# Kernel tuning notes

Hardware: AMD Instinct MI355X
Metric: run time of the kernel (lower is better)

The kernel has to match this reference:

```python
import jax, jax.numpy as jnp
import numpy as np

N, E, HN, K = 4096, 8192, 1024, 8
NF, EF = 128, 64
NH = [256, 256]
EH = [64, 64]
EMB = NH[-1] + len(EH)  # 258
BN_EPS = 1e-5


def setup_inputs() -> dict:
    key = jax.random.key(0)
    ks = jax.random.split(key, 16)

    def nrm(k, shape, fan):
        return jax.random.normal(k, shape, jnp.float32) / np.float32(np.sqrt(fan))

    return {
        "X_n": jax.random.normal(ks[0], (N, NF), jnp.float32),
        "X_e": jax.random.normal(ks[1], (E, EF), jnp.float32),
        # row-normalized-ish adjacency and scaled Laplacian to keep activations bounded
        "A_tilde": jax.random.uniform(ks[2], (N, N), jnp.float32) / np.float32(N),
        "L1_tilde": jax.random.normal(ks[3], (E, E), jnp.float32) / np.float32(np.sqrt(E)),
        "B1": jax.random.normal(ks[4], (N, E), jnp.float32) / np.float32(np.sqrt(E)),
        # GNN params (Linear stores weight as [out, in])
        "gnn_W1": nrm(ks[5], (NH[0], NF), NF), "gnn_b1": jnp.zeros((NH[0],), jnp.float32),
        "gnn_W2": nrm(ks[6], (NH[1], NH[0]), NH[0]), "gnn_b2": jnp.zeros((NH[1],), jnp.float32),
        # HoSC layer 1: in=EF, out=EH[0]
        "hosc_W1": nrm(ks[7], (EH[0], EF), EF), "hosc_b1": jnp.zeros((EH[0],), jnp.float32),
        "bn1_g": jnp.ones((EH[0],), jnp.float32), "bn1_b": jnp.zeros((EH[0],), jnp.float32),
        # HoSC layer 2: in=1 (after channel-max), out=EH[1]
        "hosc_W2": nrm(ks[8], (EH[1], 1), 1), "hosc_b2": jnp.zeros((EH[1],), jnp.float32),
        "bn2_g": jnp.ones((EH[1],), jnp.float32), "bn2_b": jnp.zeros((EH[1],), jnp.float32),
        # heads
        "node_W": nrm(ks[9], (1, EMB), EMB), "node_b": jnp.zeros((1,), jnp.float32),
        "edge_W": nrm(ks[10], (1, len(EH)), len(EH)), "edge_b": jnp.zeros((1,), jnp.float32),
        "hyper_W": nrm(ks[11], (1, EMB), EMB), "hyper_b": jnp.zeros((1,), jnp.float32),
        "hyperedges": jax.random.randint(ks[12], (HN, K), 0, N, jnp.int64),
    }


def _bn(x, g, b):
    # training-mode BatchNorm1d: biased batch statistics over rows
    m = jnp.mean(x, axis=0)
    v = jnp.var(x, axis=0)
    return g * (x - m) / jnp.sqrt(v + BN_EPS) + b


def _hosc_layer(Z, L1, W, bias, g, b):
    Zt = Z @ W.T + bias            # [E, out]
    Zc = L1 @ Zt                   # [E, out]
    Zp = jax.nn.relu(_bn(Zc, g, b))
    return jnp.max(Zp, axis=1, keepdims=True)  # [E, 1]


def reference(X_n, X_e, A_tilde, L1_tilde, B1,
              gnn_W1, gnn_b1, gnn_W2, gnn_b2,
              hosc_W1, hosc_b1, bn1_g, bn1_b,
              hosc_W2, hosc_b2, bn2_g, bn2_b,
              node_W, node_b, edge_W, edge_b, hyper_W, hyper_b,
              hyperedges):
    # --- GNN over nodes ---
    H = jax.nn.relu((A_tilde @ X_n) @ gnn_W1.T + gnn_b1)   # [N, 256]
    H_n = jax.nn.relu((A_tilde @ H) @ gnn_W2.T + gnn_b2)   # [N, 256]

    # --- HoSC over edges ---
    Z1 = _hosc_layer(X_e, L1_tilde, hosc_W1, hosc_b1, bn1_g, bn1_b)  # [E, 1]
    Z2 = _hosc_layer(Z1, L1_tilde, hosc_W2, hosc_b2, bn2_g, bn2_b)   # [E, 1]
    Z_H = jnp.concatenate([Z1, Z2], axis=1)                 # [E, 2]

    # --- fuse edge info into nodes ---
    H_e = B1 @ Z_H                                          # [N, 2]
    Hcat = jnp.concatenate([H_n, H_e], axis=1)              # [N, 258]

    node_prob = jax.nn.sigmoid(Hcat @ node_W.T + node_b).squeeze(-1)  # [N]
    edge_prob = jax.nn.sigmoid(Z_H @ edge_W.T + edge_b).squeeze(-1)   # [E]

    # vectorized hyperedge gather-mean-linear-sigmoid (fixed-size hyperedges)
    hfeat = Hcat[hyperedges].mean(axis=1)                   # [HN, 258]
    hyperedge_prob = jax.nn.sigmoid(hfeat @ hyper_W.T + hyper_b)  # [HN, 1]

    return node_prob, edge_prob, hyperedge_prob, Hcat
```

## Files before the change

### kernel.cpp

```cpp
#include <hip/hip_runtime.h>
#include <hip/hip_bf16.h>

using f32x4  = __attribute__((ext_vector_type(4))) float;
using u32x4  = __attribute__((ext_vector_type(4))) unsigned int;
using bf16x8 = __attribute__((ext_vector_type(8))) short;

__device__ __forceinline__ ushort f2bf(float x) {
    union { __hip_bfloat16 h; ushort u; } cv;
    cv.h = __float2bfloat16(x);
    return cv.u;
}
__device__ __forceinline__ unsigned pk2(float lo, float hi) {
    return (unsigned)f2bf(lo) | ((unsigned)f2bf(hi) << 16);
}
__device__ __forceinline__ float bflo(unsigned u) {
    union { unsigned i; float f; } c; c.i = u << 16; return c.f;
}
__device__ __forceinline__ float bfhi(unsigned u) {
    union { unsigned i; float f; } c; c.i = u & 0xFFFF0000u; return c.f;
}
__device__ __forceinline__ float sigmoidf_(float x) { return 1.f / (1.f + expf(-x)); }

template<bool A_BF16, bool SPLIT, bool RELU, bool BF16_OUT, bool HAS_BIAS>
__global__ __launch_bounds__(256)
void gemm_kernel(const void* __restrict__ Avoid, const ushort* __restrict__ B,
                 const float* __restrict__ bias, float* __restrict__ Cf,
                 ushort* __restrict__ Cb, int M, int N, int K, int ldc, int kPerChunk)
{
    __shared__ ushort As[128 * 40];
    __shared__ ushort Bs[64 * 40];
    const int tid  = threadIdx.x;
    const int lane = tid & 63;
    const int wid  = tid >> 6;
    const int wr   = wid >> 1, wc = wid & 1;
    const int g    = lane >> 4, lr = lane & 15;
    const long m0  = (long)blockIdx.x * 128;
    const int  n0  = blockIdx.y * 64;

    int kbeg = 0, kend = K;
    if (SPLIT) { kbeg = blockIdx.z * kPerChunk; kend = kbeg + kPerChunk; if (kend > K) kend = K; }

    const int bkr = tid & 31;
    const int bcb = tid >> 5;

    const float*  Af = (const float*)Avoid;
    const ushort* Ab = (const ushort*)Avoid;

    f32x4 pa[4];
    u32x4 pab[2];
    u32x4 pb;

    auto loadT = [&](int k0) {
        if (A_BF16) {
#pragma unroll
            for (int i = 0; i < 2; i++) {
                int s = tid + 256 * i; int row = s >> 2, c8 = s & 3;
                pab[i] = *(const u32x4*)(Ab + (m0 + row) * (long)K + k0 + c8 * 8);
            }
        } else {
#pragma unroll
            for (int i = 0; i < 4; i++) {
                int s = tid + 256 * i; int row = s >> 3, c4 = s & 7;
                pa[i] = *(const f32x4*)(Af + (m0 + row) * (long)K + k0 + c4 * 4);
            }
        }
        pb = *(const u32x4*)(B + (long)(k0 + bkr) * N + n0 + bcb * 8);
    };
    auto storeT = [&]() {
        if (A_BF16) {
#pragma unroll
            for (int i = 0; i < 2; i++) {
                int s = tid + 256 * i; int row = s >> 2, c8 = s & 3;
                *(u32x4*)(&As[row * 40 + c8 * 8]) = pab[i];
            }
        } else {
#pragma unroll
            for (int i = 0; i < 4; i++) {
                int s = tid + 256 * i; int row = s >> 3, c4 = s & 7;
                ushort4 w;
                w.x = f2bf(pa[i].x); w.y = f2bf(pa[i].y);
                w.z = f2bf(pa[i].z); w.w = f2bf(pa[i].w);
                *(ushort4*)(&As[row * 40 + c4 * 4]) = w;
            }
        }
        const ushort* p8 = (const ushort*)&pb;
#pragma unroll
        for (int j = 0; j < 8; j++) Bs[(bcb * 8 + j) * 40 + bkr] = p8[j];
    };

    f32x4 acc[4][2] = {};

    const int nk = (kend - kbeg) >> 5;
    loadT(kbeg);
    for (int t = 0; t < nk; ++t) {
        storeT();
        __syncthreads();
        if (t + 1 < nk) loadT(kbeg + ((t + 1) << 5));
        bf16x8 af[4], bfr[2];
#pragma unroll
        for (int fm = 0; fm < 4; fm++)
            af[fm] = *(const bf16x8*)(&As[(wr * 64 + fm * 16 + lr) * 40 + g * 8]);
#pragma unroll
        for (int fn = 0; fn < 2; fn++)
            bfr[fn] = *(const bf16x8*)(&Bs[(wc * 32 + fn * 16 + lr) * 40 + g * 8]);
#pragma unroll
        for (int fm = 0; fm < 4; fm++)
#pragma unroll
            for (int fn = 0; fn < 2; fn++)
                acc[fm][fn] = __builtin_amdgcn_mfma_f32_16x16x32_bf16(af[fm], bfr[fn], acc[fm][fn], 0, 0, 0);
        __syncthreads();
    }

    if (SPLIT) {
        float* P = Cf + (long)blockIdx.z * M * N;
#pragma unroll
        for (int fm = 0; fm < 4; fm++)
#pragma unroll
            for (int fn = 0; fn < 2; fn++)
#pragma unroll
                for (int rr = 0; rr < 4; rr++) {
                    long row = m0 + wr * 64 + fm * 16 + g * 4 + rr;
                    int  col = n0 + wc * 32 + fn * 16 + lr;
                    P[row * N + col] = acc[fm][fn][rr];
                }
    } else {
#pragma unroll
        for (int fm = 0; fm < 4; fm++)
#pragma unroll
            for (int fn = 0; fn < 2; fn++)
#pragma unroll
                for (int rr = 0; rr < 4; rr++) {
                    long row = m0 + wr * 64 + fm * 16 + g * 4 + rr;
                    int  col = n0 + wc * 32 + fn * 16 + lr;
                    float v = acc[fm][fn][rr];
                    if (HAS_BIAS) v += bias[col];
                    if (RELU) v = fmaxf(v, 0.f);
                    if (BF16_OUT) Cb[row * ldc + col] = f2bf(v);
                    else          Cf[row * ldc + col] = v;
                }
    }
}

__global__ __launch_bounds__(256) void reduce_add_bf16(const float* __restrict__ P,
                                                       ushort* __restrict__ C, int MN, int nz)
{
    int i = blockIdx.x * 256 + threadIdx.x;
    int n4 = MN >> 2;
    if (i >= n4) return;
    f32x4 a = ((const f32x4*)P)[i];
    for (int z = 1; z < nz; z++) a += ((const f32x4*)(P + (long)z * MN))[i];
    ushort4 o; o.x = f2bf(a.x); o.y = f2bf(a.y); o.z = f2bf(a.z); o.w = f2bf(a.w);
    ((ushort4*)C)[i] = o;
}

__global__ __launch_bounds__(256) void prep_k(const float* __restrict__ L1, ushort* __restrict__ L1b,
                                              const float* __restrict__ A, ushort* __restrict__ Abf,
                                              const float* __restrict__ Xn, ushort* __restrict__ Xnb,
                                              const float* __restrict__ W1, ushort* __restrict__ W1t,
                                              const float* __restrict__ W2, ushort* __restrict__ W2t,
                                              const float* __restrict__ Wh, ushort* __restrict__ Wht,
                                              float* __restrict__ stats)
{
    int b = blockIdx.x, t = threadIdx.x;
    if (b < 32768) {
        long j = (long)b * 256 + t;
        f32x4 v0 = ((const f32x4*)L1)[2 * j];
        f32x4 v1 = ((const f32x4*)L1)[2 * j + 1];
        u32x4 w;
        w.x = pk2(v0.x, v0.y); w.y = pk2(v0.z, v0.w);
        w.z = pk2(v1.x, v1.y); w.w = pk2(v1.z, v1.w);
        ((u32x4*)L1b)[j] = w;
    } else if (b < 40960) {
        long j = (long)(b - 32768) * 256 + t;
        f32x4 v0 = ((const f32x4*)A)[2 * j];
        f32x4 v1 = ((const f32x4*)A)[2 * j + 1];
        u32x4 w;
        w.x = pk2(v0.x, v0.y); w.y = pk2(v0.z, v0.w);
        w.z = pk2(v1.x, v1.y); w.w = pk2(v1.z, v1.w);
        ((u32x4*)Abf)[j] = w;
    } else if (b < 41216) {
        long j = (long)(b - 40960) * 256 + t;
        f32x4 v0 = ((const f32x4*)Xn)[2 * j];
        f32x4 v1 = ((const f32x4*)Xn)[2 * j + 1];
        u32x4 w;
        w.x = pk2(v0.x, v0.y); w.y = pk2(v0.z, v0.w);
        w.z = pk2(v1.x, v1.y); w.w = pk2(v1.z, v1.w);
        ((u32x4*)Xnb)[j] = w;
    } else if (b < 41344) {
        int j = (b - 41216) * 256 + t;
        int i = j >> 8, o = j & 255;
        W1t[j] = f2bf(W1[o * 128 + i]);
    } else if (b < 41600) {
        int j = (b - 41344) * 256 + t;
        int i = j >> 8, o = j & 255;
        W2t[j] = f2bf(W2[o * 256 + i]);
    } else if (b < 41616) {
        int j = (b - 41600) * 256 + t;
        int i = j >> 6, o = j & 63;
        Wht[j] = f2bf(Wh[o * 64 + i]);
    } else {
        if (t < 192) stats[t] = 0.f;
    }
}

__global__ __launch_bounds__(256) void bnred_k(const float* __restrict__ P,
                                               float* __restrict__ Zc,
                                               float* __restrict__ gsum, float* __restrict__ gsq)
{
    const long MN = 8192 * 64;
    int b = blockIdx.x, t = threadIdx.x;
    int c = t & 63, rg = t >> 6;
    float sx = 0.f, sq = 0.f;
    int base = b * 32 + rg;
#pragma unroll 4
    for (int i = 0; i < 8; i++) {
        long idx = (long)(base + 4 * i) * 64 + c;
        float x = 0.f;
#pragma unroll
        for (int z = 0; z < 8; z++) x += P[idx + z * MN];
        Zc[idx] = x;
        sx += x; sq += x * x;
    }
    __shared__ float ls[256], lq[256];
    ls[t] = sx; lq[t] = sq;
    __syncthreads();
    if (t < 64) {
        float a = ls[t] + ls[t + 64] + ls[t + 128] + ls[t + 192];
        float q = lq[t] + lq[t + 64] + lq[t + 128] + lq[t + 192];
        atomicAdd(&gsum[t], a);
        atomicAdd(&gsq[t], q);
    }
}

__global__ __launch_bounds__(256) void z1_k(const float* __restrict__ Zc,
                                            const float* __restrict__ gsum, const float* __restrict__ gsq,
                                            const float* __restrict__ g, const float* __restrict__ b,
                                            float* __restrict__ Z1)
{
    int w = threadIdx.x >> 6, lane = threadIdx.x & 63;
    int row = blockIdx.x * 4 + w;
    const float inv = 1.f / 8192.f;
    float m = gsum[lane] * inv;
    float v = gsq[lane] * inv - m * m;
    float x = Zc[row * 64 + lane];
    float y = fmaxf(g[lane] * (x - m) * rsqrtf(v + 1e-5f) + b[lane], 0.f);
#pragma unroll
    for (int o = 32; o > 0; o >>= 1) y = fmaxf(y, __shfl_xor(y, o));
    if (lane == 0) Z1[row] = y;
}

__global__ __launch_bounds__(256) void pass2_k(const ushort* __restrict__ L1b, const float* __restrict__ Z1,
                                               float* __restrict__ s, float* __restrict__ r)
{
    int row = blockIdx.x, t = threadIdx.x;
    int l = t & 63, w = t >> 6;
    const u32x4* rp = (const u32x4*)(L1b + (long)row * 8192);
    const f32x4* z4 = (const f32x4*)Z1;
    float as = 0.f, ar = 0.f;
#pragma unroll 2
    for (int k = 0; k < 4; k++) {
        int j = t + 256 * k;
        u32x4 v = rp[j];
        f32x4 za = z4[2 * j], zb = z4[2 * j + 1];
        float x0 = bflo(v.x), x1 = bfhi(v.x);
        float x2 = bflo(v.y), x3 = bfhi(v.y);
        float x4 = bflo(v.z), x5 = bfhi(v.z);
        float x6 = bflo(v.w), x7 = bfhi(v.w);
        as += x0 * za.x + x1 * za.y + x2 * za.z + x3 * za.w
            + x4 * zb.x + x5 * zb.y + x6 * zb.z + x7 * zb.w;
        ar += x0 + x1 + x2 + x3 + x4 + x5 + x6 + x7;
    }
#pragma unroll
    for (int o = 32; o > 0; o >>= 1) { as += __shfl_xor(as, o); ar += __shfl_xor(ar, o); }
    __shared__ float sw[4], rw[4];
    if (l == 0) { sw[w] = as; rw[w] = ar; }
    __syncthreads();
    if (t == 0) {
        s[row] = sw[0] + sw[1] + sw[2] + sw[3];
        r[row] = rw[0] + rw[1] + rw[2] + rw[3];
    }
}

__global__ __launch_bounds__(256) void stats2_k(const float* __restrict__ s, const float* __restrict__ r,
                                                float* __restrict__ S5)
{
    int t = threadIdx.x, l = t & 63, w = t >> 6;
    float Ss = 0, Sr = 0, Sss = 0, Srr = 0, Ssr = 0;
    for (int i = t; i < 8192; i += 256) {
        float sv = s[i], rv = r[i];
        Ss += sv; Sr += rv; Sss += sv * sv; Srr += rv * rv; Ssr += sv * rv;
    }
#pragma unroll
    for (int o = 32; o > 0; o >>= 1) {
        Ss += __shfl_xor(Ss, o); Sr += __shfl_xor(Sr, o);
        Sss += __shfl_xor(Sss, o); Srr += __shfl_xor(Srr, o); Ssr += __shfl_xor(Ssr, o);
    }
    __shared__ float buf[4][5];
    if (l == 0) { buf[w][0] = Ss; buf[w][1] = Sr; buf[w][2] = Sss; buf[w][3] = Srr; buf[w][4] = Ssr; }
    __syncthreads();
    if (t < 5) S5[t] = buf[0][t] + buf[1][t] + buf[2][t] + buf[3][t];
}

__global__ __launch_bounds__(256) void z2_edge_k(const float* __restrict__ s, const float* __restrict__ r,
                                                 const float* __restrict__ S,
                                                 const float* __restrict__ W2, const float* __restrict__ b2,
                                                 const float* __restrict__ g2, const float* __restrict__ bb2,
                                                 const float* __restrict__ eW, const float* __restrict__ eb,
                                                 const float* __restrict__ Z1,
                                                 float* __restrict__ Z2, float* __restrict__ edge_out)
{
    int w = threadIdx.x >> 6, lane = threadIdx.x & 63;
    int row = blockIdx.x * 4 + w;
    const float inv = 1.f / 8192.f;
    float ms = S[0] * inv, mr = S[1] * inv;
    float vs = S[2] * inv - ms * ms;
    float vr = S[3] * inv - mr * mr;
    float cv = S[4] * inv - ms * mr;
    float w2 = W2[lane], bz = b2[lane];
    float mc = w2 * ms + bz * mr;
    float vc = w2 * w2 * vs + 2.f * w2 * bz * cv + bz * bz * vr;
    float x  = w2 * s[row] + bz * r[row];
    float y  = fmaxf(g2[lane] * (x - mc) * rsqrtf(vc + 1e-5f) + bb2[lane], 0.f);
#pragma unroll
    for (int o = 32; o > 0; o >>= 1) y = fmaxf(y, __shfl_xor(y, o));
    if (lane == 0) {
        Z2[row] = y;
        float e = Z1[row] * eW[0] + y * eW[1] + eb[0];
        edge_out[row] = sigmoidf_(e);
    }
}

__global__ __launch_bounds__(256) void he_node_k(const float* __restrict__ B1, const float* __restrict__ Z1,
                                                 const float* __restrict__ Z2, float* __restrict__ hcat,
                                                 const float* __restrict__ nW, const float* __restrict__ nb,
                                                 float* __restrict__ node_out)
{
    int n = blockIdx.x, t = threadIdx.x;
    int l = t & 63, w = t >> 6;
    const f32x4* rp  = (const f32x4*)(B1 + (long)n * 8192);
    const f32x4* z1v = (const f32x4*)Z1;
    const f32x4* z2v = (const f32x4*)Z2;
    float a1 = 0.f, a2 = 0.f;
#pragma unroll 4
    for (int k = 0; k < 8; k++) {
        f32x4 v = rp[t + 256 * k];
        f32x4 p = z1v[t + 256 * k];
        f32x4 q = z2v[t + 256 * k];
        a1 += v.x * p.x + v.y * p.y + v.z * p.z + v.w * p.w;
        a2 += v.x * q.x + v.y * q.y + v.z * q.z + v.w * q.w;
    }
    float d = hcat[(long)n * 258 + t] * nW[t];
#pragma unroll
    for (int o = 32; o > 0; o >>= 1) {
        a1 += __shfl_xor(a1, o); a2 += __shfl_xor(a2, o); d += __shfl_xor(d, o);
    }
    __shared__ float s1[4], s2[4], s3[4];
    if (l == 0) { s1[w] = a1; s2[w] = a2; s3[w] = d; }
    __syncthreads();
    if (t == 0) {
        float A1 = s1[0] + s1[1] + s1[2] + s1[3];
        float A2 = s2[0] + s2[1] + s2[2] + s2[3];
        float D  = s3[0] + s3[1] + s3[2] + s3[3];
        hcat[(long)n * 258 + 256] = A1;
        hcat[(long)n * 258 + 257] = A2;
        node_out[n] = sigmoidf_(D + A1 * nW[256] + A2 * nW[257] + nb[0]);
    }
}

__global__ __launch_bounds__(256) void hyper_k(const void* __restrict__ he_idx,
                                               const float* __restrict__ hcat,
                                               const float* __restrict__ hW, const float* __restrict__ hb,
                                               float* __restrict__ out)
{
    int w = threadIdx.x >> 6, lane = threadIdx.x & 63;
    int h = blockIdx.x * 4 + w;
    const unsigned int* u = (const unsigned int*)he_idx;
    unsigned int odd = u[2 * lane + 1];
    bool is64 = __all(odd == 0u);
    float acc = 0.f;
    for (int k = 0; k < 8; k++) {
        int idx;
        if (is64) idx = (int)((const long long*)he_idx)[h * 8 + k];
        else      idx = ((const int*)he_idx)[h * 8 + k];
        const float* hr = hcat + (long)idx * 258;
        for (int d = lane; d < 258; d += 64) acc += hr[d] * hW[d];
    }
    acc *= 0.125f;
#pragma unroll
    for (int o = 32; o > 0; o >>= 1) acc += __shfl_xor(acc, o);
    if (lane == 0) out[h] = sigmoidf_(acc + hb[0]);
}

extern "C" void kernel_launch(void* const* d_in, const int* in_sizes, int n_in,
                              void* d_out, int out_size, void* d_ws, size_t ws_size,
                              hipStream_t stream)
{
    const float* X_n  = (const float*)d_in[0];
    const float* X_e  = (const float*)d_in[1];
    const float* A_t  = (const float*)d_in[2];
    const float* L1   = (const float*)d_in[3];
    const float* B1   = (const float*)d_in[4];
    const float* gW1  = (const float*)d_in[5];
    const float* gb1  = (const float*)d_in[6];
    const float* gW2  = (const float*)d_in[7];
    const float* gb2  = (const float*)d_in[8];
    const float* hW1  = (const float*)d_in[9];
    const float* hb1  = (const float*)d_in[10];
    const float* bn1g = (const float*)d_in[11];
    const float* bn1b = (const float*)d_in[12];
    const float* hW2  = (const float*)d_in[13];
    const float* hb2  = (const float*)d_in[14];
    const float* bn2g = (const float*)d_in[15];
    const float* bn2b = (const float*)d_in[16];
    const float* nW   = (const float*)d_in[17];
    const float* nb   = (const float*)d_in[18];
    const float* eW   = (const float*)d_in[19];
    const float* ebb  = (const float*)d_in[20];
    const float* yW   = (const float*)d_in[21];
    const float* yb   = (const float*)d_in[22];
    const void*  he   = d_in[23];

    float* out       = (float*)d_out;
    float* out_node  = out;
    float* out_edge  = out + 4096;
    float* out_hyper = out + 12288;
    float* hcat      = out + 13312;

    size_t off = 0;
    auto alloc = [&](size_t bytes) {
        void* p = (char*)d_ws + off;
        off = (off + bytes + 255) & ~(size_t)255;
        return p;
    };
    ushort* L1bf  = (ushort*)alloc((size_t)8192 * 8192 * 2);
    ushort* Abf   = (ushort*)alloc((size_t)4096 * 4096 * 2);
    ushort* Xn_bf = (ushort*)alloc(4096 * 128 * 2);
    ushort* W1t   = (ushort*)alloc(128 * 256 * 2);
    ushort* W2t   = (ushort*)alloc(256 * 256 * 2);
    ushort* W1ht  = (ushort*)alloc(64 * 64 * 2);
    ushort* C1b   = (ushort*)alloc(4096 * 128 * 2);
    ushort* H_bf  = (ushort*)alloc(4096 * 256 * 2);
    ushort* C2b   = (ushort*)alloc(4096 * 256 * 2);
    ushort* Zt1   = (ushort*)alloc(8192 * 64 * 2);
    float*  Zc1   = (float*)alloc(8192 * 64 * 4);
    float*  stats = (float*)alloc(256 * 4);
    float*  gsum  = stats;
    float*  gsq   = stats + 64;
    float*  S5    = stats + 128;
    float*  Z1    = (float*)alloc(8192 * 4);
    float*  Z2    = (float*)alloc(8192 * 4);
    float*  sbuf  = (float*)alloc(8192 * 4);
    float*  rbuf  = (float*)alloc(8192 * 4);
    float*  P     = (float*)alloc((size_t)8192 * 64 * 8 * 4);

    prep_k<<<41617, 256, 0, stream>>>(L1, L1bf, A_t, Abf, X_n, Xn_bf,
                                      gW1, W1t, gW2, W2t, hW1, W1ht, stats);

    gemm_kernel<true, true, false, false, false><<<dim3(32, 2, 4), 256, 0, stream>>>(
        Abf, Xn_bf, nullptr, P, nullptr, 4096, 128, 4096, 128, 1024);
    reduce_add_bf16<<<512, 256, 0, stream>>>(P, C1b, 4096 * 128, 4);
    gemm_kernel<true, false, true, true, true><<<dim3(32, 4, 1), 256, 0, stream>>>(
        C1b, W1t, gb1, nullptr, H_bf, 4096, 256, 128, 256, 0);
    gemm_kernel<true, true, false, false, false><<<dim3(32, 4, 2), 256, 0, stream>>>(
        Abf, H_bf, nullptr, P, nullptr, 4096, 256, 4096, 256, 2048);
    reduce_add_bf16<<<1024, 256, 0, stream>>>(P, C2b, 4096 * 256, 2);
    gemm_kernel<true, false, true, false, true><<<dim3(32, 4, 1), 256, 0, stream>>>(
        C2b, W2t, gb2, hcat, nullptr, 4096, 256, 256, 258, 0);

    gemm_kernel<false, false, false, true, true><<<dim3(64, 1, 1), 256, 0, stream>>>(
        X_e, W1ht, hb1, nullptr, Zt1, 8192, 64, 64, 64, 0);
    gemm_kernel<true, true, false, false, false><<<dim3(64, 1, 8), 256, 0, stream>>>(
        L1bf, Zt1, nullptr, P, nullptr, 8192, 64, 8192, 64, 1024);
    bnred_k<<<256, 256, 0, stream>>>(P, Zc1, gsum, gsq);
    z1_k<<<2048, 256, 0, stream>>>(Zc1, gsum, gsq, bn1g, bn1b, Z1);

    pass2_k<<<8192, 256, 0, stream>>>(L1bf, Z1, sbuf, rbuf);
    stats2_k<<<1, 256, 0, stream>>>(sbuf, rbuf, S5);
    z2_edge_k<<<2048, 256, 0, stream>>>(sbuf, rbuf, S5, hW2, hb2, bn2g, bn2b,
                                        eW, ebb, Z1, Z2, out_edge);

    he_node_k<<<4096, 256, 0, stream>>>(B1, Z1, Z2, hcat, nW, nb, out_node);
    hyper_k<<<256, 256, 0, stream>>>(he, hcat, yW, yb, out_hyper);
}
```

Measured before the change: 297.1 us.

## Fuse fp32-to-bf16 conversion of A and L1 into first GEMM loads

The separate conversion pass over the large fp32 A_tilde and L1_tilde matrices is removed from the prep kernel. The first GEMM that consumes each matrix now reads fp32 directly, converts it in registers, and has the blockIdx.y==0 blocks write the bf16 copy for later reuse (second A GEMM, pass2). This drops one full read of each large fp32 matrix, in exchange for fp32 loads inside the GEMM and redundant conversion across the N-tile blocks. stats2_k is also widened from 256 to 1024 threads.

```diff
diff --git a/kernel.cpp b/kernel.cpp
--- a/kernel.cpp
+++ b/kernel.cpp
@@ -21,11 +21,12 @@
 }
 __device__ __forceinline__ float sigmoidf_(float x) { return 1.f / (1.f + expf(-x)); }
 
-template<bool A_BF16, bool SPLIT, bool RELU, bool BF16_OUT, bool HAS_BIAS>
+template<bool A_BF16, bool AOUT, bool SPLIT, bool RELU, bool BF16_OUT, bool HAS_BIAS>
 __global__ __launch_bounds__(256)
 void gemm_kernel(const void* __restrict__ Avoid, const ushort* __restrict__ B,
                  const float* __restrict__ bias, float* __restrict__ Cf,
-                 ushort* __restrict__ Cb, int M, int N, int K, int ldc, int kPerChunk)
+                 ushort* __restrict__ Cb, ushort* __restrict__ Aout,
+                 int M, int N, int K, int ldc, int kPerChunk)
 {
     __shared__ ushort As[128 * 40];
     __shared__ ushort Bs[64 * 40];
@@ -45,6 +46,7 @@
 
     const float*  Af = (const float*)Avoid;
     const ushort* Ab = (const ushort*)Avoid;
+    const bool doAout = AOUT && (blockIdx.y == 0);
 
     f32x4 pa[4];
     u32x4 pab[2];
@@ -66,7 +68,7 @@
         }
         pb = *(const u32x4*)(B + (long)(k0 + bkr) * N + n0 + bcb * 8);
     };
-    auto storeT = [&]() {
+    auto storeT = [&](int k0) {
         if (A_BF16) {
 #pragma unroll
             for (int i = 0; i < 2; i++) {
@@ -81,6 +83,10 @@
                 w.x = f2bf(pa[i].x); w.y = f2bf(pa[i].y);
                 w.z = f2bf(pa[i].z); w.w = f2bf(pa[i].w);
                 *(ushort4*)(&As[row * 40 + c4 * 4]) = w;
+                if (AOUT) {
+                    if (doAout)
+                        *(ushort4*)(Aout + (m0 + row) * (long)K + k0 + c4 * 4) = w;
+                }
             }
         }
         const ushort* p8 = (const ushort*)&pb;
@@ -93,7 +99,7 @@
     const int nk = (kend - kbeg) >> 5;
     loadT(kbeg);
     for (int t = 0; t < nk; ++t) {
-        storeT();
+        storeT(kbeg + (t << 5));
         __syncthreads();
         if (t + 1 < nk) loadT(kbeg + ((t + 1) << 5));
         bf16x8 af[4], bfr[2];
@@ -153,49 +159,31 @@
     ((ushort4*)C)[i] = o;
 }
 
-__global__ __launch_bounds__(256) void prep_k(const float* __restrict__ L1, ushort* __restrict__ L1b,
-                                              const float* __restrict__ A, ushort* __restrict__ Abf,
-                                              const float* __restrict__ Xn, ushort* __restrict__ Xnb,
+__global__ __launch_bounds__(256) void prep_k(const float* __restrict__ Xn, ushort* __restrict__ Xnb,
                                               const float* __restrict__ W1, ushort* __restrict__ W1t,
                                               const float* __restrict__ W2, ushort* __restrict__ W2t,
                                               const float* __restrict__ Wh, ushort* __restrict__ Wht,
                                               float* __restrict__ stats)
 {
     int b = blockIdx.x, t = threadIdx.x;
-    if (b < 32768) {
+    if (b < 256) {
         long j = (long)b * 256 + t;
-        f32x4 v0 = ((const f32x4*)L1)[2 * j];
-        f32x4 v1 = ((const f32x4*)L1)[2 * j + 1];
-        u32x4 w;
-        w.x = pk2(v0.x, v0.y); w.y = pk2(v0.z, v0.w);
-        w.z = pk2(v1.x, v1.y); w.w = pk2(v1.z, v1.w);
-        ((u32x4*)L1b)[j] = w;
-    } else if (b < 40960) {
-        long j = (long)(b - 32768) * 256 + t;
-        f32x4 v0 = ((const f32x4*)A)[2 * j];
-        f32x4 v1 = ((const f32x4*)A)[2 * j + 1];
-        u32x4 w;
-        w.x = pk2(v0.x, v0.y); w.y = pk2(v0.z, v0.w);
-        w.z = pk2(v1.x, v1.y); w.w = pk2(v1.z, v1.w);
-        ((u32x4*)Abf)[j] = w;
-    } else if (b < 41216) {
-        long j = (long)(b - 40960) * 256 + t;
         f32x4 v0 = ((const f32x4*)Xn)[2 * j];
         f32x4 v1 = ((const f32x4*)Xn)[2 * j + 1];
         u32x4 w;
         w.x = pk2(v0.x, v0.y); w.y = pk2(v0.z, v0.w);
         w.z = pk2(v1.x, v1.y); w.w = pk2(v1.z, v1.w);
         ((u32x4*)Xnb)[j] = w;
-    } else if (b < 41344) {
-        int j = (b - 41216) * 256 + t;
+    } else if (b < 384) {
+        int j = (b - 256) * 256 + t;
         int i = j >> 8, o = j & 255;
         W1t[j] = f2bf(W1[o * 128 + i]);
-    } else if (b < 41600) {
-        int j = (b - 41344) * 256 + t;
+    } else if (b < 640) {
+        int j = (b - 384) * 256 + t;
         int i = j >> 8, o = j & 255;
         W2t[j] = f2bf(W2[o * 256 + i]);
-    } else if (b < 41616) {
-        int j = (b - 41600) * 256 + t;
+    } else if (b < 656) {
+        int j = (b - 640) * 256 + t;
         int i = j >> 6, o = j & 63;
         Wht[j] = f2bf(Wh[o * 64 + i]);
     } else {
@@ -281,12 +269,12 @@
     }
 }
 
-__global__ __launch_bounds__(256) void stats2_k(const float* __restrict__ s, const float* __restrict__ r,
-                                                float* __restrict__ S5)
+__global__ __launch_bounds__(1024) void stats2_k(const float* __restrict__ s, const float* __restrict__ r,
+                                                 float* __restrict__ S5)
 {
     int t = threadIdx.x, l = t & 63, w = t >> 6;
     float Ss = 0, Sr = 0, Sss = 0, Srr = 0, Ssr = 0;
-    for (int i = t; i < 8192; i += 256) {
+    for (int i = t; i < 8192; i += 1024) {
         float sv = s[i], rv = r[i];
         Ss += sv; Sr += rv; Sss += sv * sv; Srr += rv * rv; Ssr += sv * rv;
     }
@@ -295,10 +283,15 @@
         Ss += __shfl_xor(Ss, o); Sr += __shfl_xor(Sr, o);
         Sss += __shfl_xor(Sss, o); Srr += __shfl_xor(Srr, o); Ssr += __shfl_xor(Ssr, o);
     }
-    __shared__ float buf[4][5];
+    __shared__ float buf[16][5];
     if (l == 0) { buf[w][0] = Ss; buf[w][1] = Sr; buf[w][2] = Sss; buf[w][3] = Srr; buf[w][4] = Ssr; }
     __syncthreads();
-    if (t < 5) S5[t] = buf[0][t] + buf[1][t] + buf[2][t] + buf[3][t];
+    if (t < 5) {
+        float a = 0.f;
+#pragma unroll
+        for (int i = 0; i < 16; i++) a += buf[i][t];
+        S5[t] = a;
+    }
 }
 
 __global__ __launch_bounds__(256) void z2_edge_k(const float* __restrict__ s, const float* __restrict__ r,
@@ -453,29 +446,28 @@
     float*  rbuf  = (float*)alloc(8192 * 4);
     float*  P     = (float*)alloc((size_t)8192 * 64 * 8 * 4);
 
-    prep_k<<<41617, 256, 0, stream>>>(L1, L1bf, A_t, Abf, X_n, Xn_bf,
-                                      gW1, W1t, gW2, W2t, hW1, W1ht, stats);
-
-    gemm_kernel<true, true, false, false, false><<<dim3(32, 2, 4), 256, 0, stream>>>(
-        Abf, Xn_bf, nullptr, P, nullptr, 4096, 128, 4096, 128, 1024);
+    prep_k<<<657, 256, 0, stream>>>(X_n, Xn_bf, gW1, W1t, gW2, W2t, hW1, W1ht, stats);
+
+    gemm_kernel<false, true, true, false, false, false><<<dim3(32, 2, 4), 256, 0, stream>>>(
+        A_t, Xn_bf, nullptr, P, nullptr, Abf, 4096, 128, 4096, 128, 1024);
     reduce_add_bf16<<<512, 256, 0, stream>>>(P, C1b, 4096 * 128, 4);
-    gemm_kernel<true, false, true, true, true><<<dim3(32, 4, 1), 256, 0, stream>>>(
-        C1b, W1t, gb1, nullptr, H_bf, 4096, 256, 128, 256, 0);
-    gemm_kernel<true, true, false, false, false><<<dim3(32, 4, 2), 256, 0, stream>>>(
-        Abf, H_bf, nullptr, P, nullptr, 4096, 256, 4096, 256, 2048);
+    gemm_kernel<true, false, false, true, true, true><<<dim3(32, 4, 1), 256, 0, stream>>>(
+        C1b, W1t, gb1, nullptr, H_bf, nullptr, 4096, 256, 128, 256, 0);
+    gemm_kernel<true, false, true, false, false, false><<<dim3(32, 4, 2), 256, 0, stream>>>(
+        Abf, H_bf, nullptr, P, nullptr, nullptr, 4096, 256, 4096, 256, 2048);
     reduce_add_bf16<<<1024, 256, 0, stream>>>(P, C2b, 4096 * 256, 2);
-    gemm_kernel<true, false, true, false, true><<<dim3(32, 4, 1), 256, 0, stream>>>(
-        C2b, W2t, gb2, hcat, nullptr, 4096, 256, 256, 258, 0);
-
-    gemm_kernel<false, false, false, true, true><<<dim3(64, 1, 1), 256, 0, stream>>>(
-        X_e, W1ht, hb1, nullptr, Zt1, 8192, 64, 64, 64, 0);
-    gemm_kernel<true, true, false, false, false><<<dim3(64, 1, 8), 256, 0, stream>>>(
-        L1bf, Zt1, nullptr, P, nullptr, 8192, 64, 8192, 64, 1024);
+    gemm_kernel<true, false, false, true, false, true><<<dim3(32, 4, 1), 256, 0, stream>>>(
+        C2b, W2t, gb2, hcat, nullptr, nullptr, 4096, 256, 256, 258, 0);
+
+    gemm_kernel<false, false, false, false, true, true><<<dim3(64, 1, 1), 256, 0, stream>>>(
+        X_e, W1ht, hb1, nullptr, Zt1, nullptr, 8192, 64, 64, 64, 0);
+    gemm_kernel<false, true, true, false, false, false><<<dim3(64, 1, 8), 256, 0, stream>>>(
+        L1, Zt1, nullptr, P, nullptr, L1bf, 8192, 64, 8192, 64, 1024);
     bnred_k<<<256, 256, 0, stream>>>(P, Zc1, gsum, gsq);
     z1_k<<<2048, 256, 0, stream>>>(Zc1, gsum, gsq, bn1g, bn1b, Z1);
 
     pass2_k<<<8192, 256, 0, stream>>>(L1bf, Z1, sbuf, rbuf);
-    stats2_k<<<1, 256, 0, stream>>>(sbuf, rbuf, S5);
+    stats2_k<<<1, 1024, 0, stream>>>(sbuf, rbuf, S5);
     z2_edge_k<<<2048, 256, 0, stream>>>(sbuf, rbuf, S5, hW2, hb2, bn2g, bn2b,
                                         eW, ebb, Z1, Z2, out_edge);
 
```

Result: slower. 325.9 us (+9.7%).
